# Optimization experiments

Hardware: AMD Instinct MI355X
Metric: run time of the kernel (lower is better)

Reference implementation:

```python
import jax, jax.numpy as jnp
import numpy as np

HEADS = 8
DIM_HEAD = 64
SCALE = DIM_HEAD ** -0.5


def setup_inputs() -> dict:
    key = jax.random.key(0)
    ks = jax.random.split(key, 5)
    dim, hidden = 512, HEADS * DIM_HEAD
    b, l = 4, 2048
    return {
        "x": jax.random.normal(ks[0], (b, dim, l), jnp.float32),
        "w_qkv": jax.random.normal(ks[1], (3 * hidden, dim), jnp.float32) * 0.02,
        "b_qkv": jax.random.normal(ks[2], (3 * hidden,), jnp.float32) * 0.02,
        "w_out": jax.random.normal(ks[3], (dim, hidden), jnp.float32) * 0.02,
        "b_out": jax.random.normal(ks[4], (dim,), jnp.float32) * 0.02,
    }


def reference(x, w_qkv, b_qkv, w_out, b_out):
    b, c, l = x.shape
    # Conv1d kernel-size-1 == per-position linear: (b, 3*hidden, l)
    qkv = jnp.einsum('oc,bcl->bol', w_qkv, x) + b_qkv[None, :, None]
    q, k, v = jnp.split(qkv, 3, axis=1)
    # rearrange 'b (h d) l -> b h d l'
    def split_heads(t):
        return t.reshape(b, HEADS, DIM_HEAD, l)
    q, k, v = split_heads(q) * SCALE, split_heads(k), split_heads(v)
    sim = jnp.einsum('bhdi,bhdj->bhij', q, k)  # [b,h,l,l]
    sim = sim - jax.lax.stop_gradient(jnp.max(sim, axis=-1, keepdims=True))
    attn = jax.nn.softmax(sim, axis=-1)
    out = jnp.einsum('bhij,bhdj->bhid', attn, v)  # [b,h,l,d]
    # 'b h l d -> b (h d) l'
    out = out.transpose(0, 1, 3, 2).reshape(b, HEADS * DIM_HEAD, l)
    out = jnp.einsum('oc,bcl->bol', w_out, out) + b_out[None, :, None]
    return out
```

## Files before the change

### kernel.cpp

```cpp
#include <hip/hip_runtime.h>
#include <hip/hip_bf16.h>

#define B 4
#define DIM 512
#define HID 512
#define NH 8
#define DH 64
#define L 2048
#define QSCALE (0.125f * 1.4426950408889634f)

typedef __attribute__((ext_vector_type(8)))  short bf16x8;
typedef __attribute__((ext_vector_type(4)))  float f32x4;
typedef __attribute__((ext_vector_type(16))) float f32x16;
typedef __attribute__((ext_vector_type(4)))  int   i32x4;

static __device__ __forceinline__ short f32_to_bf16s(float f) {
    __hip_bfloat16 h = __float2bfloat16(f);
    return *reinterpret_cast<short*>(&h);
}
static __device__ __forceinline__ float bf16s_to_f32(short s) {
    return __uint_as_float(((unsigned)(unsigned short)s) << 16);
}

static __device__ __forceinline__ float fast_exp2(float x) {
    float r;
    asm("v_exp_f32 %0, %1" : "=v"(r) : "v"(x));
    return r;
}

static __device__ __forceinline__ void gl_lds16(const short* g, short* l) {
    __builtin_amdgcn_global_load_lds(
        (const __attribute__((address_space(1))) void*)g,
        (__attribute__((address_space(3))) void*)l, 16, 0, 0);
}

static __device__ __forceinline__ bf16x8 lds_frag(const short* t, int row, int c) {
    bf16x8 v;
    __builtin_memcpy(&v, t + row * 64 + ((c ^ (row & 7)) * 8), 16);
    return v;
}

__global__ __launch_bounds__(256) void prep(
    const float* __restrict__ wq, const float* __restrict__ wo,
    short* __restrict__ wdst,
    const float* __restrict__ X, short* __restrict__ XT)
{
    const int bx  = blockIdx.x;
    const int tid = threadIdx.x;
    if (bx < 1024) {
        const int i = (bx * 256 + tid) * 4;
        float4 v;
        if (i < 786432) v = *(const float4*)(wq + i);
        else            v = *(const float4*)(wo + (i - 786432));
        short4 pk = {f32_to_bf16s(v.x), f32_to_bf16s(v.y),
                     f32_to_bf16s(v.z), f32_to_bf16s(v.w)};
        *(short4*)(wdst + i) = pk;
        return;
    }
    const int bid = bx - 1024;
    const int l0 = (bid & 31) * 64;
    const int c0 = ((bid >> 5) & 7) * 64;
    const int b  = bid >> 8;

    __shared__ float tile[64][65];
    const float* Xb = X + (size_t)b * DIM * L;

    #pragma unroll
    for (int it = 0; it < 16; ++it) {
        const int cr = (tid >> 6) + it * 4;
        const int lc = tid & 63;
        tile[cr][lc] = Xb[(size_t)(c0 + cr) * L + l0 + lc];
    }
    __syncthreads();
    short* XTb = XT + (size_t)b * L * DIM;
    #pragma unroll
    for (int it = 0; it < 8; ++it) {
        const int l  = (tid >> 5) + it * 8;
        const int c2 = (tid & 31) * 2;
        short2 pk = {f32_to_bf16s(tile[c2][l]), f32_to_bf16s(tile[c2 + 1][l])};
        *(short2*)(XTb + (size_t)(l0 + l) * DIM + c0 + c2) = pk;
    }
}

__global__ __launch_bounds__(256) void qkv_mfma(
    const short* __restrict__ Wb, const short* __restrict__ XT,
    const float* __restrict__ bias,
    short* __restrict__ qws, short* __restrict__ kws, short* __restrict__ vws)
{
    const int lBase = blockIdx.x * 128;
    const int oBase = blockIdx.y * 128;
    const int b     = blockIdx.z;
    const int tid   = threadIdx.x;
    const int wave  = tid >> 6;
    const int lane  = tid & 63;
    const int lid   = lane & 15;
    const int quad  = lane >> 4;
    const int rsub  = lane >> 3;
    const int cl    = (lane & 7) ^ rsub;

    __shared__ __align__(16) short Wt[128 * 64];
    __shared__ __align__(16) short Xt[128 * 64];

    const short* XTb = XT + (size_t)b * L * DIM;
    const int oLoc = (wave & 1) * 64;
    const int lLoc = (wave >> 1) * 64;

    f32x4 acc[4][4];
    #pragma unroll
    for (int mi = 0; mi < 4; ++mi)
        #pragma unroll
        for (int ni = 0; ni < 4; ++ni) acc[mi][ni] = (f32x4){0.f, 0.f, 0.f, 0.f};

    for (int c0 = 0; c0 < DIM; c0 += 64) {
        if (c0) __syncthreads();
        #pragma unroll
        for (int t = 0; t < 4; ++t) {
            const int ch = wave * 4 + t;
            const int r  = ch * 8 + rsub;
            gl_lds16(Wb  + (size_t)(oBase + r) * DIM + c0 + cl * 8, Wt + ch * 512);
            gl_lds16(XTb + (size_t)(lBase + r) * DIM + c0 + cl * 8, Xt + ch * 512);
        }
        __syncthreads();
        #pragma unroll
        for (int kc = 0; kc < 2; ++kc) {
            bf16x8 a[4], bb[4];
            #pragma unroll
            for (int mi = 0; mi < 4; ++mi)
                a[mi] = lds_frag(Wt, oLoc + mi * 16 + lid, kc * 4 + quad);
            #pragma unroll
            for (int ni = 0; ni < 4; ++ni)
                bb[ni] = lds_frag(Xt, lLoc + ni * 16 + lid, kc * 4 + quad);
            #pragma unroll
            for (int mi = 0; mi < 4; ++mi)
                #pragma unroll
                for (int ni = 0; ni < 4; ++ni)
                    acc[mi][ni] = __builtin_amdgcn_mfma_f32_16x16x32_bf16(
                        a[mi], bb[ni], acc[mi][ni], 0, 0, 0);
        }
    }

    const int rty = oBase >> 9;
    const float sc = (rty == 0) ? QSCALE : 1.0f;
    const int h = ((oBase + oLoc) >> 6) & 7;

    #pragma unroll
    for (int mi = 0; mi < 4; ++mi) {
        const int dB = mi * 16 + quad * 4;
        float bia[4];
        #pragma unroll
        for (int r = 0; r < 4; ++r)
            bia[r] = bias[oBase + oLoc + mi * 16 + quad * 4 + r];

        if (rty < 2) {
            short* dst = (rty == 0 ? qws : kws) + (((size_t)b * NH + h) * L) * DH;
            #pragma unroll
            for (int ni = 0; ni < 4; ++ni) {
                const int l = lBase + lLoc + ni * 16 + lid;
                short4 pk = {f32_to_bf16s((acc[mi][ni][0] + bia[0]) * sc),
                             f32_to_bf16s((acc[mi][ni][1] + bia[1]) * sc),
                             f32_to_bf16s((acc[mi][ni][2] + bia[2]) * sc),
                             f32_to_bf16s((acc[mi][ni][3] + bia[3]) * sc)};
                *(short4*)(dst + (size_t)l * DH + dB) = pk;
            }
        } else {
            short* dst = vws + (((size_t)b * NH + h) * DH) * L;
            #pragma unroll
            for (int r = 0; r < 4; ++r) {
                const int d = dB + r;
                #pragma unroll
                for (int ni = 0; ni < 4; ++ni)
                    dst[(size_t)d * L + lBase + lLoc + ni * 16 + lid] =
                        f32_to_bf16s((acc[mi][ni][r] + bia[r]) * sc);
            }
        }
    }
}

__global__ __launch_bounds__(256) void attn_mfma(
    const short* __restrict__ Q, const short* __restrict__ K,
    const short* __restrict__ VT,
    short* __restrict__ Op0, short* __restrict__ Op1,
    short* __restrict__ Op2, short* __restrict__ Op3,
    float* __restrict__ Lp)
{
    const int iTile = blockIdx.x;
    const int h     = blockIdx.y;
    const int b     = blockIdx.z >> 2;
    const int qtr   = blockIdx.z & 3;
    const int tid   = threadIdx.x;
    const int wave  = tid >> 6;
    const int lane  = tid & 63;
    const int l5    = lane & 31;
    const int me    = lane >> 5;
    const int rsub  = lane >> 3;
    const int cl    = (lane & 7) ^ rsub;

    short* __restrict__ Op = (qtr & 2) ? ((qtr & 1) ? Op3 : Op2)
                                       : ((qtr & 1) ? Op1 : Op0);
    float* __restrict__ Lq = Lp + (size_t)qtr * (B * NH * L);

    const size_t headOff = ((size_t)b * NH + h) * (size_t)L * DH;
    const short* Qh = Q + headOff;
    const short* Kh = K + headOff;
    const short* Vh = VT + headOff;

    __shared__ __align__(16) short Kt[64 * 64];
    __shared__ __align__(16) short Vt[64 * 64];

    const int q0 = iTile * 128 + wave * 32;
    bf16x8 qf[4];
    #pragma unroll
    for (int kc = 0; kc < 4; ++kc)
        qf[kc] = *(const bf16x8*)(Qh + (size_t)(q0 + l5) * DH + kc * 16 + me * 8);

    f32x16 oacc[2];
    #pragma unroll
    for (int dt = 0; dt < 2; ++dt)
        #pragma unroll
        for (int r = 0; r < 16; ++r) oacc[dt][r] = 0.f;
    float lsum = 0.f;

    const int jt0 = qtr * 8;
    for (int it = 0; it < 8; ++it) {
        const int j0 = (jt0 + it) * 64;
        if (it) __syncthreads();
        #pragma unroll
        for (int t = 0; t < 2; ++t) {
            const int ch = wave * 2 + t;
            const int r  = ch * 8 + rsub;
            gl_lds16(Kh + (size_t)(j0 + r) * DH + cl * 8, Kt + ch * 512);
            gl_lds16(Vh + (size_t)r * L + j0 + cl * 8,    Vt + ch * 512);
        }
        __syncthreads();

        bf16x8 pf[4];
        #pragma unroll
        for (int mt = 0; mt < 2; ++mt) {
            f32x16 s;
            #pragma unroll
            for (int r = 0; r < 16; ++r) s[r] = 0.f;
            #pragma unroll
            for (int kc = 0; kc < 4; ++kc) {
                bf16x8 a = lds_frag(Kt, mt * 32 + l5, kc * 2 + me);
                s = __builtin_amdgcn_mfma_f32_32x32x16_bf16(a, qf[kc], s, 0, 0, 0);
            }
            unsigned dw[4][2];
            #pragma unroll
            for (int g = 0; g < 4; ++g) {
                #pragma unroll
                for (int p = 0; p < 2; ++p) {
                    const float p0 = fast_exp2(s[4 * g + 2 * p]);
                    const float p1 = fast_exp2(s[4 * g + 2 * p + 1]);
                    const unsigned pk = __builtin_amdgcn_perm(
                        __float_as_uint(p1), __float_as_uint(p0), 0x07060302u);
                    lsum += __uint_as_float(pk << 16);
                    lsum += __uint_as_float(pk & 0xffff0000u);
                    dw[g][p] = pk;
                }
            }
            #pragma unroll
            for (int kl = 0; kl < 2; ++kl) {
                const unsigned own0 = me ? dw[2 * kl + 1][0] : dw[2 * kl][0];
                const unsigned own1 = me ? dw[2 * kl + 1][1] : dw[2 * kl][1];
                const unsigned snd0 = me ? dw[2 * kl][0] : dw[2 * kl + 1][0];
                const unsigned snd1 = me ? dw[2 * kl][1] : dw[2 * kl + 1][1];
                const unsigned rcv0 = (unsigned)__shfl_xor((int)snd0, 32);
                const unsigned rcv1 = (unsigned)__shfl_xor((int)snd1, 32);
                i32x4 bi;
                bi[0] = (int)(me ? rcv0 : own0);
                bi[1] = (int)(me ? rcv1 : own1);
                bi[2] = (int)(me ? own0 : rcv0);
                bi[3] = (int)(me ? own1 : rcv1);
                pf[mt * 2 + kl] = __builtin_bit_cast(bf16x8, bi);
            }
        }

        #pragma unroll
        for (int kc = 0; kc < 4; ++kc) {
            #pragma unroll
            for (int dt = 0; dt < 2; ++dt) {
                bf16x8 a = lds_frag(Vt, dt * 32 + l5, kc * 2 + me);
                oacc[dt] = __builtin_amdgcn_mfma_f32_32x32x16_bf16(a, pf[kc], oacc[dt], 0, 0, 0);
            }
        }
    }

    const float vh = lsum + __shfl_xor(lsum, 32);
    const int qg = q0 + l5;
    if (me == 0)
        Lq[((size_t)b * NH + h) * L + qg] = vh;

    const float inv = 1.0f / vh;
    short* ab = Op + ((size_t)b * L + qg) * HID + h * DH;
    #pragma unroll
    for (int dt = 0; dt < 2; ++dt) {
        #pragma unroll
        for (int g = 0; g < 4; ++g) {
            const int d = dt * 32 + 8 * g + 4 * me;
            short4 pk = {f32_to_bf16s(oacc[dt][4 * g]     * inv),
                         f32_to_bf16s(oacc[dt][4 * g + 1] * inv),
                         f32_to_bf16s(oacc[dt][4 * g + 2] * inv),
                         f32_to_bf16s(oacc[dt][4 * g + 3] * inv)};
            *(short4*)(ab + d) = pk;
        }
    }
}

__global__ __launch_bounds__(256) void combine4(
    const short* __restrict__ O0, const short* __restrict__ O1,
    const short* __restrict__ O2, const short* __restrict__ O3,
    const float* __restrict__ Lp, short* __restrict__ Abf)
{
    const int g = blockIdx.x * 256 + threadIdx.x;
    const int i = g * 4;
    const int b = i >> 20;
    const int rem = i & 1048575;
    const int l = rem >> 9;
    const int c = rem & 511;
    const int h = c >> 6;
    const size_t li = ((size_t)b * NH + h) * L + l;
    const float w0 = Lp[li];
    const float w1 = Lp[li + (size_t)B * NH * L];
    const float w2 = Lp[li + (size_t)2 * B * NH * L];
    const float w3 = Lp[li + (size_t)3 * B * NH * L];
    const float inv = 1.0f / (w0 + w1 + w2 + w3);
    const short4 a = *(const short4*)(O0 + i);
    const short4 bb = *(const short4*)(O1 + i);
    const short4 cc = *(const short4*)(O2 + i);
    const short4 dd = *(const short4*)(O3 + i);
    short4 pk = {
        f32_to_bf16s((w0 * bf16s_to_f32(a.x) + w1 * bf16s_to_f32(bb.x) +
                      w2 * bf16s_to_f32(cc.x) + w3 * bf16s_to_f32(dd.x)) * inv),
        f32_to_bf16s((w0 * bf16s_to_f32(a.y) + w1 * bf16s_to_f32(bb.y) +
                      w2 * bf16s_to_f32(cc.y) + w3 * bf16s_to_f32(dd.y)) * inv),
        f32_to_bf16s((w0 * bf16s_to_f32(a.z) + w1 * bf16s_to_f32(bb.z) +
                      w2 * bf16s_to_f32(cc.z) + w3 * bf16s_to_f32(dd.z)) * inv),
        f32_to_bf16s((w0 * bf16s_to_f32(a.w) + w1 * bf16s_to_f32(bb.w) +
                      w2 * bf16s_to_f32(cc.w) + w3 * bf16s_to_f32(dd.w)) * inv)};
    *(short4*)(Abf + i) = pk;
}

__global__ __launch_bounds__(256) void out_mfma(
    const short* __restrict__ Wo, const short* __restrict__ Abf,
    const float* __restrict__ bias, float* __restrict__ out)
{
    const int lBase = blockIdx.x * 128;
    const int oBase = blockIdx.y * 64;
    const int b     = blockIdx.z;
    const int tid   = threadIdx.x;
    const int wave  = tid >> 6;
    const int lane  = tid & 63;
    const int lid   = lane & 15;
    const int quad  = lane >> 4;
    const int rsub  = lane >> 3;
    const int cl    = (lane & 7) ^ rsub;

    __shared__ __align__(16) short Wt[64 * 64];
    __shared__ __align__(16) short At[128 * 64];

    const short* Ab = Abf + (size_t)b * L * HID;
    const int oLoc = (wave & 1) * 32;
    const int lLoc = (wave >> 1) * 64;

    f32x4 acc[2][4];
    #pragma unroll
    for (int mi = 0; mi < 2; ++mi)
        #pragma unroll
        for (int ni = 0; ni < 4; ++ni) acc[mi][ni] = (f32x4){0.f, 0.f, 0.f, 0.f};

    for (int c0 = 0; c0 < HID; c0 += 64) {
        if (c0) __syncthreads();
        #pragma unroll
        for (int t = 0; t < 2; ++t) {
            const int ch = wave * 2 + t;
            const int r  = ch * 8 + rsub;
            gl_lds16(Wo + (size_t)(oBase + r) * HID + c0 + cl * 8, Wt + ch * 512);
        }
        #pragma unroll
        for (int t = 0; t < 4; ++t) {
            const int ch = wave * 4 + t;
            const int r  = ch * 8 + rsub;
            gl_lds16(Ab + (size_t)(lBase + r) * HID + c0 + cl * 8, At + ch * 512);
        }
        __syncthreads();
        #pragma unroll
        for (int kc = 0; kc < 2; ++kc) {
            bf16x8 a[2], bb[4];
            #pragma unroll
            for (int mi = 0; mi < 2; ++mi)
                a[mi] = lds_frag(Wt, oLoc + mi * 16 + lid, kc * 4 + quad);
            #pragma unroll
            for (int ni = 0; ni < 4; ++ni)
                bb[ni] = lds_frag(At, lLoc + ni * 16 + lid, kc * 4 + quad);
            #pragma unroll
            for (int mi = 0; mi < 2; ++mi)
                #pragma unroll
                for (int ni = 0; ni < 4; ++ni)
                    acc[mi][ni] = __builtin_amdgcn_mfma_f32_16x16x32_bf16(
                        a[mi], bb[ni], acc[mi][ni], 0, 0, 0);
        }
    }

    #pragma unroll
    for (int mi = 0; mi < 2; ++mi) {
        #pragma unroll
        for (int r = 0; r < 4; ++r) {
            const int o = oBase + oLoc + mi * 16 + quad * 4 + r;
            const float bia = bias[o];
            #pragma unroll
            for (int ni = 0; ni < 4; ++ni)
                out[((size_t)b * DIM + o) * L + lBase + lLoc + ni * 16 + lid] =
                    acc[mi][ni][r] + bia;
        }
    }
}

extern "C" void kernel_launch(void* const* d_in, const int* in_sizes, int n_in,
                              void* d_out, int out_size, void* d_ws, size_t ws_size,
                              hipStream_t stream)
{
    const float* x     = (const float*)d_in[0];
    const float* w_qkv = (const float*)d_in[1];
    const float* b_qkv = (const float*)d_in[2];
    const float* w_out = (const float*)d_in[3];
    const float* b_out = (const float*)d_in[4];
    float* out = (float*)d_out;

    char* w = (char*)d_ws;
    short* xT  = (short*)(w);
    short* wqb = (short*)(w + (8u << 20));
    short* wob = wqb + 786432;
    short* qws = (short*)(w + (10u << 20));
    short* kws = (short*)(w + (18u << 20));
    short* vws = (short*)(w + (26u << 20));
    short* Abf = (short*)(w + (34u << 20));
    short* Op1 = (short*)(w);
    short* Op2 = (short*)(w + (42u << 20));
    short* Op3 = (short*)(w + (50u << 20));
    float* Lp  = (float*)(w + (58u << 20));
    short* Op0 = (short*)d_out;

    dim3 blk(256);
    prep<<<dim3(2048), blk, 0, stream>>>(w_qkv, w_out, wqb, x, xT);
    qkv_mfma<<<dim3(L / 128, 1536 / 128, B), blk, 0, stream>>>(
        wqb, xT, b_qkv, qws, kws, vws);
    attn_mfma<<<dim3(L / 128, NH, B * 4), blk, 0, stream>>>(
        qws, kws, vws, Op0, Op1, Op2, Op3, Lp);
    combine4<<<dim3(4096), blk, 0, stream>>>(Op0, Op1, Op2, Op3, Lp, Abf);
    out_mfma<<<dim3(L / 128, DIM / 64, B), blk, 0, stream>>>(
        wob, Abf, b_out, out);
}
```

Measured before the change: 165.5 us.

## Compute softmax row sums with MFMA and drop cross-half P shuffles

Result: slower. 170.0 us (+2.7%).

```diff
diff --git a/kernel.cpp b/kernel.cpp
--- a/kernel.cpp
+++ b/kernel.cpp
@@ -38,6 +38,15 @@
     bf16x8 v;
     __builtin_memcpy(&v, t + row * 64 + ((c ^ (row & 7)) * 8), 16);
     return v;
+}
+
+static __device__ __forceinline__ bf16x8 lds_vfrag(const short* t, int row,
+                                                   int c0, int me4) {
+    int2 a, b;
+    __builtin_memcpy(&a, t + row * 64 + ((c0 ^ (row & 7)) * 8 + me4), 8);
+    __builtin_memcpy(&b, t + row * 64 + (((c0 + 1) ^ (row & 7)) * 8 + me4), 8);
+    i32x4 v = {a.x, a.y, b.x, b.y};
+    return __builtin_bit_cast(bf16x8, v);
 }
 
 __global__ __launch_bounds__(256) void prep(
@@ -183,15 +192,16 @@
     short* __restrict__ Op2, short* __restrict__ Op3,
     float* __restrict__ Lp)
 {
-    const int iTile = blockIdx.x;
-    const int h     = blockIdx.y;
-    const int b     = blockIdx.z >> 2;
-    const int qtr   = blockIdx.z & 3;
+    const int h     = blockIdx.x >> 2;
+    const int qtr   = blockIdx.x & 3;
+    const int b     = blockIdx.y;
+    const int iTile = blockIdx.z;
     const int tid   = threadIdx.x;
     const int wave  = tid >> 6;
     const int lane  = tid & 63;
     const int l5    = lane & 31;
     const int me    = lane >> 5;
+    const int me4   = me * 4;
     const int rsub  = lane >> 3;
     const int cl    = (lane & 7) ^ rsub;
 
@@ -211,14 +221,18 @@
     bf16x8 qf[4];
     #pragma unroll
     for (int kc = 0; kc < 4; ++kc)
-        qf[kc] = *(const bf16x8*)(Qh + (size_t)(q0 + l5) * DH + kc * 16 + me * 8);
-
-    f32x16 oacc[2];
+        qf[kc] = *(const bf16x8*)(Qh + (size_t)(q0 + l5) * DH + kc * 16 + me4 * 2);
+
+    const i32x4 onesI = {0x3F803F80, 0x3F803F80, 0x3F803F80, 0x3F803F80};
+    const bf16x8 ones = __builtin_bit_cast(bf16x8, onesI);
+
+    f32x16 oacc[2], lacc;
     #pragma unroll
     for (int dt = 0; dt < 2; ++dt)
         #pragma unroll
         for (int r = 0; r < 16; ++r) oacc[dt][r] = 0.f;
-    float lsum = 0.f;
+    #pragma unroll
+    for (int r = 0; r < 16; ++r) lacc[r] = 0.f;
 
     const int jt0 = qtr * 8;
     for (int it = 0; it < 8; ++it) {
@@ -233,7 +247,7 @@
         }
         __syncthreads();
 
-        bf16x8 pf[4];
+        unsigned dw[2][4][2];
         #pragma unroll
         for (int mt = 0; mt < 2; ++mt) {
             f32x16 s;
@@ -244,48 +258,37 @@
                 bf16x8 a = lds_frag(Kt, mt * 32 + l5, kc * 2 + me);
                 s = __builtin_amdgcn_mfma_f32_32x32x16_bf16(a, qf[kc], s, 0, 0, 0);
             }
-            unsigned dw[4][2];
             #pragma unroll
             for (int g = 0; g < 4; ++g) {
                 #pragma unroll
                 for (int p = 0; p < 2; ++p) {
                     const float p0 = fast_exp2(s[4 * g + 2 * p]);
                     const float p1 = fast_exp2(s[4 * g + 2 * p + 1]);
-                    const unsigned pk = __builtin_amdgcn_perm(
+                    dw[mt][g][p] = __builtin_amdgcn_perm(
                         __float_as_uint(p1), __float_as_uint(p0), 0x07060302u);
-                    lsum += __uint_as_float(pk << 16);
-                    lsum += __uint_as_float(pk & 0xffff0000u);
-                    dw[g][p] = pk;
                 }
             }
+        }
+
+        #pragma unroll
+        for (int mt = 0; mt < 2; ++mt) {
             #pragma unroll
             for (int kl = 0; kl < 2; ++kl) {
-                const unsigned own0 = me ? dw[2 * kl + 1][0] : dw[2 * kl][0];
-                const unsigned own1 = me ? dw[2 * kl + 1][1] : dw[2 * kl][1];
-                const unsigned snd0 = me ? dw[2 * kl][0] : dw[2 * kl + 1][0];
-                const unsigned snd1 = me ? dw[2 * kl][1] : dw[2 * kl + 1][1];
-                const unsigned rcv0 = (unsigned)__shfl_xor((int)snd0, 32);
-                const unsigned rcv1 = (unsigned)__shfl_xor((int)snd1, 32);
-                i32x4 bi;
-                bi[0] = (int)(me ? rcv0 : own0);
-                bi[1] = (int)(me ? rcv1 : own1);
-                bi[2] = (int)(me ? own0 : rcv0);
-                bi[3] = (int)(me ? own1 : rcv1);
-                pf[mt * 2 + kl] = __builtin_bit_cast(bf16x8, bi);
+                i32x4 bi = {(int)dw[mt][2 * kl][0], (int)dw[mt][2 * kl][1],
+                            (int)dw[mt][2 * kl + 1][0], (int)dw[mt][2 * kl + 1][1]};
+                bf16x8 pb = __builtin_bit_cast(bf16x8, bi);
+                lacc = __builtin_amdgcn_mfma_f32_32x32x16_bf16(ones, pb, lacc, 0, 0, 0);
+                const int c0 = mt * 4 + kl * 2;
+                #pragma unroll
+                for (int dt = 0; dt < 2; ++dt) {
+                    bf16x8 a = lds_vfrag(Vt, dt * 32 + l5, c0, me4);
+                    oacc[dt] = __builtin_amdgcn_mfma_f32_32x32x16_bf16(a, pb, oacc[dt], 0, 0, 0);
+                }
             }
         }
-
-        #pragma unroll
-        for (int kc = 0; kc < 4; ++kc) {
-            #pragma unroll
-            for (int dt = 0; dt < 2; ++dt) {
-                bf16x8 a = lds_frag(Vt, dt * 32 + l5, kc * 2 + me);
-                oacc[dt] = __builtin_amdgcn_mfma_f32_32x32x16_bf16(a, pf[kc], oacc[dt], 0, 0, 0);
-            }
-        }
-    }
-
-    const float vh = lsum + __shfl_xor(lsum, 32);
+    }
+
+    const float vh = lacc[0];
     const int qg = q0 + l5;
     if (me == 0)
         Lq[((size_t)b * NH + h) * L + qg] = vh;
@@ -296,7 +299,7 @@
     for (int dt = 0; dt < 2; ++dt) {
         #pragma unroll
         for (int g = 0; g < 4; ++g) {
-            const int d = dt * 32 + 8 * g + 4 * me;
+            const int d = dt * 32 + 8 * g + me4;
             short4 pk = {f32_to_bf16s(oacc[dt][4 * g]     * inv),
                          f32_to_bf16s(oacc[dt][4 * g + 1] * inv),
                          f32_to_bf16s(oacc[dt][4 * g + 2] * inv),
@@ -444,7 +447,7 @@
     prep<<<dim3(2048), blk, 0, stream>>>(w_qkv, w_out, wqb, x, xT);
     qkv_mfma<<<dim3(L / 128, 1536 / 128, B), blk, 0, stream>>>(
         wqb, xT, b_qkv, qws, kws, vws);
-    attn_mfma<<<dim3(L / 128, NH, B * 4), blk, 0, stream>>>(
+    attn_mfma<<<dim3(NH * 4, B, L / 128), blk, 0, stream>>>(
         qws, kws, vws, Op0, Op1, Op2, Op3, Lp);
     combine4<<<dim3(4096), blk, 0, stream>>>(Op0, Op1, Op2, Op3, Lp, Abf);
     out_mfma<<<dim3(L / 128, DIM / 64, B), blk, 0, stream>>>(
```
